# Optimization experiments

Hardware: AMD Instinct MI355X
Metric: run time of the kernel (lower is better)

The kernel has to match this reference:

```python
import jax, jax.numpy as jnp
import numpy as np

N = 100000   # total nodes in batch
E = 200000   # total edges
G = 4000     # number of graphs
H = 128      # gin_size = gin_hidden = gin_mlp_hidden = linear_hidden
L = 2        # gin_layers


def setup_inputs() -> dict:
    key = jax.random.key(0)
    ks = jax.random.split(key, 24)
    rn = lambda i, shape, s=0.05: (jax.random.normal(ks[i], shape, jnp.float32) * s)
    inp = dict(
        x=rn(0, (N, 14), 1.0),
        edge_attr=rn(1, (E, 4), 1.0),
        edge_index=jax.random.randint(ks[2], (2, E), 0, N, dtype=jnp.int32),
        batch=jnp.sort(jax.random.randint(ks[3], (N,), 0, G, dtype=jnp.int32)),
        node_w=rn(4, (14, H)), node_b=jnp.zeros((H,), jnp.float32),
        edge_w=rn(5, (4, H)), edge_b=jnp.zeros((H,), jnp.float32),
        eps=jnp.zeros((L,), jnp.float32),
        gin_w1=rn(6, (L, H, H)), gin_b1=jnp.zeros((L, H), jnp.float32),
        gin_w2=rn(7, (L, H, H)), gin_b2=jnp.zeros((L, H), jnp.float32),
        em_w1=rn(8, (L, H, H)), em_b1=jnp.zeros((L, H), jnp.float32),
        em_w2=rn(9, (L, H, H)), em_b2=jnp.zeros((L, H), jnp.float32),
        gru_wih=rn(10, (3 * H, H)), gru_whh=rn(11, (3 * H, H)),
        gru_bih=jnp.zeros((3 * H,), jnp.float32), gru_bhh=jnp.zeros((3 * H,), jnp.float32),
        lstm_wih=rn(12, (4 * H, 2 * H)), lstm_whh=rn(13, (4 * H, H)),
        lstm_bih=jnp.zeros((4 * H,), jnp.float32), lstm_bhh=jnp.zeros((4 * H,), jnp.float32),
        fc_w1=rn(14, (2 * H, H)), fc_b1=jnp.zeros((H,), jnp.float32),
        fc_w2=rn(15, (H, 1)), fc_b2=jnp.zeros((1,), jnp.float32),
    )
    return inp


def reference(x, edge_attr, edge_index, batch,
              node_w, node_b, edge_w, edge_b, eps,
              gin_w1, gin_b1, gin_w2, gin_b2,
              em_w1, em_b1, em_w2, em_b2,
              gru_wih, gru_whh, gru_bih, gru_bhh,
              lstm_wih, lstm_whh, lstm_bih, lstm_bhh,
              fc_w1, fc_b1, fc_w2, fc_b2):
    src, dst = edge_index[0], edge_index[1]
    node = x @ node_w + node_b          # [N,H]
    edge = edge_attr @ edge_w + edge_b  # [E,H]
    h = node                            # GRU hidden state
    for l in range(L):
        # GINEConv: msg = relu(x_src + e), scatter-add to dst, (1+eps)*x + agg, then MLP
        msg = jax.nn.relu(node[src] + edge)                     # [E,H] gather
        agg = jax.ops.segment_sum(msg, dst, num_segments=N)     # [N,H] scatter-add
        z = (1.0 + eps[l]) * node + agg
        m = jax.nn.relu(z @ gin_w1[l] + gin_b1[l]) @ gin_w2[l] + gin_b2[l]
        # GRU cell (seq_len=1)
        gi = m @ gru_wih.T + gru_bih
        gh = h @ gru_whh.T + gru_bhh
        ir, iz, inn = jnp.split(gi, 3, axis=-1)
        hr, hz, hn = jnp.split(gh, 3, axis=-1)
        r = jax.nn.sigmoid(ir + hr)
        zt = jax.nn.sigmoid(iz + hz)
        n = jnp.tanh(inn + r * hn)
        h = (1.0 - zt) * n + zt * h
        node = h
        # edge feature update MLP
        edge = jax.nn.relu(edge @ em_w1[l] + em_b1[l]) @ em_w2[l] + em_b2[l]
    # Set2Set pooling, processing_steps=3
    qs = jnp.zeros((G, 2 * H), node.dtype)
    hl = jnp.zeros((G, H), node.dtype)
    cl = jnp.zeros((G, H), node.dtype)
    for _ in range(3):
        g = qs @ lstm_wih.T + lstm_bih + hl @ lstm_whh.T + lstm_bhh
        i_, f_, g_, o_ = jnp.split(g, 4, axis=-1)
        cl = jax.nn.sigmoid(f_) * cl + jax.nn.sigmoid(i_) * jnp.tanh(g_)
        hl = jax.nn.sigmoid(o_) * jnp.tanh(cl)
        q = hl                                                   # [G,H]
        e = jnp.sum(node * q[batch], axis=-1)                    # [N]
        emax = jax.ops.segment_max(e, batch, num_segments=G)
        ex = jnp.exp(e - emax[batch])
        denom = jax.ops.segment_sum(ex, batch, num_segments=G)
        a = ex / jnp.maximum(denom, 1e-9)[batch]                 # per-graph softmax
        r = jax.ops.segment_sum(a[:, None] * node, batch, num_segments=G)  # [G,H]
        qs = jnp.concatenate([q, r], axis=-1)                    # [G,2H]
    out = jax.nn.relu(qs @ fc_w1 + fc_b1) @ fc_w2 + fc_b2
    return out.reshape(-1)
```

## Files before the change

kernel.cpp:

```cpp
#include <hip/hip_runtime.h>
#include <hip/hip_bf16.h>

constexpr int TN = 100000;
constexpr int TE = 200000;
constexpr int TG = 4000;
constexpr int TH = 128;

using short8 = __attribute__((ext_vector_type(8))) short;
using f32x4  = __attribute__((ext_vector_type(4))) float;
typedef __hip_bfloat16 bf16;

#define DEVINL __device__ __forceinline__
DEVINL float sigm(float x)  { return 1.f / (1.f + __expf(-x)); }
DEVINL float ftanh(float x) { return 1.f - 2.f / (__expf(2.f * x) + 1.f); }
DEVINL void unpack8(uint4 v, float* f) {
    const ushort* u = (const ushort*)&v;
#pragma unroll
    for (int j = 0; j < 8; ++j) f[j] = __bfloat162float(*(const bf16*)&u[j]);
}

__global__ void convAll(const float* __restrict__ g1, const float* __restrict__ g2,
                        const float* __restrict__ e1, const float* __restrict__ e2,
                        const float* __restrict__ gwih, const float* __restrict__ gwhh,
                        const float* __restrict__ lwih, const float* __restrict__ lwhh,
                        bf16* __restrict__ w6, bf16* __restrict__ wgru,
                        bf16* __restrict__ wl) {
    int i = blockIdx.x * 256 + threadIdx.x;
    if (i < 6 * TH * TH) {
        int m = i >> 14, r = i & 16383;
        int n = r >> 7, k = r & 127;
        const float* s = (m == 0) ? g1 : (m == 1) ? g1 + TH * TH
                       : (m == 2) ? g2 : (m == 3) ? g2 + TH * TH
                       : (m == 4) ? e1 : e2;
        w6[i] = __float2bfloat16(s[k * TH + n]);
        return;
    }
    i -= 6 * TH * TH;
    if (i < 2 * 384 * TH) {
        const float* s = (i < 384 * TH) ? gwih : gwhh;
        int r = (i < 384 * TH) ? i : i - 384 * TH;
        wgru[i] = __float2bfloat16(s[r]);
        return;
    }
    i -= 2 * 384 * TH;
    if (i < 512 * 256) {
        int c = i >> 8, k = i & 255;
        float v = (k < 128) ? lwih[c * 256 + k] + lwhh[c * 128 + k] : lwih[c * 256 + k];
        wl[i] = __float2bfloat16(v);
    }
}

template<int K>
__global__ __launch_bounds__(256) void proj64(const float* __restrict__ X,
                                              const float* __restrict__ W,
                                              const float* __restrict__ b,
                                              ushort* __restrict__ out, int M) {
    __shared__ float xs[64][K];
    int tid = threadIdx.x;
    int bm = blockIdx.x * 64;
    for (int i = tid; i < 64 * K; i += 256) {
        int r = i / K, k = i % K;
        xs[r][k] = (bm + r < M) ? X[(size_t)(bm + r) * K + k] : 0.f;
    }
    __syncthreads();
    int rb = tid >> 4, h0 = (tid & 15) * 8;
    float acc[4][8];
#pragma unroll
    for (int j = 0; j < 4; ++j)
#pragma unroll
        for (int c = 0; c < 8; ++c) acc[j][c] = b[h0 + c];
#pragma unroll
    for (int k = 0; k < K; ++k) {
        float4 w0 = *(const float4*)(W + k * TH + h0);
        float4 w1 = *(const float4*)(W + k * TH + h0 + 4);
#pragma unroll
        for (int j = 0; j < 4; ++j) {
            float xv = xs[rb + 16 * j][k];
            acc[j][0] = fmaf(xv, w0.x, acc[j][0]); acc[j][1] = fmaf(xv, w0.y, acc[j][1]);
            acc[j][2] = fmaf(xv, w0.z, acc[j][2]); acc[j][3] = fmaf(xv, w0.w, acc[j][3]);
            acc[j][4] = fmaf(xv, w1.x, acc[j][4]); acc[j][5] = fmaf(xv, w1.y, acc[j][5]);
            acc[j][6] = fmaf(xv, w1.z, acc[j][6]); acc[j][7] = fmaf(xv, w1.w, acc[j][7]);
        }
    }
#pragma unroll
    for (int j = 0; j < 4; ++j) {
        int row = bm + rb + 16 * j;
        if (row >= M) continue;
        ushort o[8];
#pragma unroll
        for (int c = 0; c < 8; ++c) {
            bf16 v = __float2bfloat16(acc[j][c]);
            o[c] = *(ushort*)&v;
        }
        *(uint4*)(out + (size_t)row * TH + h0) = *(uint4*)o;
    }
}

__global__ __launch_bounds__(256) void proj_scatter(
    const float* __restrict__ X, const float* __restrict__ W,
    const float* __restrict__ b, const int* __restrict__ perm,
    ushort* __restrict__ out, int M) {
    __shared__ float xs[64][4];
    int tid = threadIdx.x;
    int bm = blockIdx.x * 64;
    if (tid < 64) {
        float4 a = make_float4(0.f, 0.f, 0.f, 0.f);
        if (bm + tid < M) a = *(const float4*)(X + (size_t)(bm + tid) * 4);
        xs[tid][0] = a.x; xs[tid][1] = a.y; xs[tid][2] = a.z; xs[tid][3] = a.w;
    }
    __syncthreads();
    int rb = tid >> 4, h0 = (tid & 15) * 8;
    float acc[4][8];
#pragma unroll
    for (int j = 0; j < 4; ++j)
#pragma unroll
        for (int c = 0; c < 8; ++c) acc[j][c] = b[h0 + c];
#pragma unroll
    for (int k = 0; k < 4; ++k) {
        float4 w0 = *(const float4*)(W + k * TH + h0);
        float4 w1 = *(const float4*)(W + k * TH + h0 + 4);
#pragma unroll
        for (int j = 0; j < 4; ++j) {
            float xv = xs[rb + 16 * j][k];
            acc[j][0] = fmaf(xv, w0.x, acc[j][0]); acc[j][1] = fmaf(xv, w0.y, acc[j][1]);
            acc[j][2] = fmaf(xv, w0.z, acc[j][2]); acc[j][3] = fmaf(xv, w0.w, acc[j][3]);
            acc[j][4] = fmaf(xv, w1.x, acc[j][4]); acc[j][5] = fmaf(xv, w1.y, acc[j][5]);
            acc[j][6] = fmaf(xv, w1.z, acc[j][6]); acc[j][7] = fmaf(xv, w1.w, acc[j][7]);
        }
    }
#pragma unroll
    for (int j = 0; j < 4; ++j) {
        int row = bm + rb + 16 * j;
        if (row >= M) continue;
        ushort o[8];
#pragma unroll
        for (int c = 0; c < 8; ++c) {
            bf16 v = __float2bfloat16(acc[j][c]);
            o[c] = *(ushort*)&v;
        }
        *(uint4*)(out + (size_t)perm[row] * TH + h0) = *(uint4*)o;
    }
}

__global__ void count_deg(const int* __restrict__ ei_dst, int* __restrict__ deg, int En) {
    int e = blockIdx.x * 256 + threadIdx.x;
    if (e < En) atomicAdd(&deg[ei_dst[e]], 1);
}
__global__ void scan_block(const int* __restrict__ deg, int* __restrict__ rowptr,
                           int* __restrict__ bsum, int Nn) {
    __shared__ int sm[256];
    int tid = threadIdx.x;
    int gid = blockIdx.x * 256 + tid;
    int v = (gid < Nn) ? deg[gid] : 0;
    int x = v;
    sm[tid] = x; __syncthreads();
    for (int off = 1; off < 256; off <<= 1) {
        int t = (tid >= off) ? sm[tid - off] : 0;
        __syncthreads();
        x += t; sm[tid] = x;
        __syncthreads();
    }
    if (gid < Nn) rowptr[gid] = x - v;
    if (tid == 255) bsum[blockIdx.x] = x;
}
__global__ void scan_bsum(const int* __restrict__ bsum, int* __restrict__ bsumx, int nb) {
    __shared__ int sm[512];
    int tid = threadIdx.x;
    int v = (tid < nb) ? bsum[tid] : 0;
    int x = v;
    sm[tid] = x; __syncthreads();
    for (int off = 1; off < 512; off <<= 1) {
        int t = (tid >= off) ? sm[tid - off] : 0;
        __syncthreads();
        x += t; sm[tid] = x;
        __syncthreads();
    }
    if (tid < nb) bsumx[tid] = x - v;
}
__global__ void add_off(int* __restrict__ rowptr, const int* __restrict__ bsumx,
                        int Nn, int Etot) {
    int gid = blockIdx.x * 256 + threadIdx.x;
    if (gid < Nn) rowptr[gid] += bsumx[gid >> 8];
    if (gid == 0) rowptr[Nn] = Etot;
}
__global__ void fill_csr(const int* __restrict__ ei_src, const int* __restrict__ ei_dst,
                         const int* __restrict__ rowptr, int* __restrict__ cur,
                         int* __restrict__ srcp, int* __restrict__ epos, int En) {
    int e = blockIdx.x * 256 + threadIdx.x;
    if (e >= En) return;
    int d = ei_dst[e];
    int p = atomicAdd(&cur[d], 1);
    int slot = rowptr[d] + p;
    srcp[slot] = ei_src[e];
    epos[e] = slot;
}
__global__ void build_gptr(const int* __restrict__ batch, int* __restrict__ gptr,
                           int Nn, int Gn) {
    int n = blockIdx.x * 256 + threadIdx.x;
    if (n >= Nn) return;
    int bc = batch[n];
    int bp = (n == 0) ? -1 : batch[n - 1];
    for (int g = bp + 1; g <= bc; ++g) gptr[g] = n;
    if (n == Nn - 1) for (int g = bc + 1; g <= Gn; ++g) gptr[g] = Nn;
}

__global__ __launch_bounds__(256) void aggregate_v8(
    const ushort* __restrict__ node, const ushort* __restrict__ ef,
    const int* __restrict__ srcp, const int* __restrict__ rowptr,
    const float* __restrict__ eps, int l, ushort* __restrict__ zb, int Nn) {
    int t = blockIdx.x * 256 + threadIdx.x;
    int n = t >> 4;
    if (n >= Nn) return;
    int c8 = (t & 15) * 8;
    float se = 1.f + eps[l];
    float acc[8];
    uint4 nv = *(const uint4*)(node + (size_t)n * TH + c8);
    unpack8(nv, acc);
#pragma unroll
    for (int j = 0; j < 8; ++j) acc[j] *= se;
    int s0 = rowptr[n], s1 = rowptr[n + 1];
    int i = s0;
    for (; i + 1 < s1; i += 2) {
        int sa = srcp[i], sb = srcp[i + 1];
        uint4 av0 = *(const uint4*)(node + (size_t)sa * TH + c8);
        uint4 bv0 = *(const uint4*)(ef + (size_t)i * TH + c8);
        uint4 av1 = *(const uint4*)(node + (size_t)sb * TH + c8);
        uint4 bv1 = *(const uint4*)(ef + (size_t)(i + 1) * TH + c8);
        float a0[8], b0[8], a1[8], b1[8];
        unpack8(av0, a0); unpack8(bv0, b0);
        unpack8(av1, a1); unpack8(bv1, b1);
#pragma unroll
        for (int j = 0; j < 8; ++j)
            acc[j] += fmaxf(a0[j] + b0[j], 0.f) + fmaxf(a1[j] + b1[j], 0.f);
    }
    if (i < s1) {
        int sa = srcp[i];
        uint4 av = *(const uint4*)(node + (size_t)sa * TH + c8);
        uint4 bv = *(const uint4*)(ef + (size_t)i * TH + c8);
        float af[8], bf[8];
        unpack8(av, af); unpack8(bv, bf);
#pragma unroll
        for (int j = 0; j < 8; ++j) acc[j] += fmaxf(af[j] + bf[j], 0.f);
    }
    ushort o[8];
#pragma unroll
    for (int j = 0; j < 8; ++j) {
        bf16 v = __float2bfloat16(acc[j]);
        o[j] = *(ushort*)&v;
    }
    *(uint4*)(zb + (size_t)n * TH + c8) = *(uint4*)o;
}

__global__ __launch_bounds__(256) void mlp2_fused(
    const ushort* __restrict__ A, const ushort* __restrict__ W1t,
    const float* __restrict__ b1, const ushort* __restrict__ W2t,
    const float* __restrict__ b2, ushort* __restrict__ C, int M)
{
    __shared__ ushort As[128 * 128];
    const int tid = threadIdx.x;
    const int bm = blockIdx.x * 128;
    const int lane = tid & 63, w = tid >> 6;
    const int lr = lane & 15, lq = lane >> 4;
    const int wm = (w & 1) * 64, wn = (w >> 1) * 64;
    short8 wf[4][4];
#pragma unroll
    for (int ni = 0; ni < 4; ++ni)
#pragma unroll
        for (int ks = 0; ks < 4; ++ks)
            wf[ni][ks] = *(const short8*)(W1t + (size_t)(wn + ni * 16 + lr) * 128 + ks * 32 + lq * 8);
#pragma unroll
    for (int p = 0; p < 8; ++p) {
        int ch = p * 256 + tid;
        int r = ch >> 4, c = ch & 15;
        int row = bm + r;
        uint4 v = make_uint4(0u, 0u, 0u, 0u);
        if (row < M) v = *(const uint4*)(A + (size_t)row * 128 + c * 8);
        *(uint4*)(&As[r * 128 + ((c ^ (r & 15)) * 8)]) = v;
    }
    __syncthreads();
    f32x4 acc[4][4] = {};
#pragma unroll
    for (int ks = 0; ks < 4; ++ks) {
        int cb = ks * 4 + lq;
        short8 af[4];
#pragma unroll
        for (int mi = 0; mi < 4; ++mi)
            af[mi] = *(const short8*)(&As[(wm + mi * 16 + lr) * 128 + ((cb ^ lr) * 8)]);
#pragma unroll
        for (int mi = 0; mi < 4; ++mi)
#pragma unroll
            for (int ni = 0; ni < 4; ++ni)
                acc[mi][ni] = __builtin_amdgcn_mfma_f32_16x16x32_bf16(af[mi], wf[ni][ks], acc[mi][ni], 0, 0, 0);
    }
    __syncthreads();
#pragma unroll
    for (int mi = 0; mi < 4; ++mi)
#pragma unroll
        for (int reg = 0; reg < 4; ++reg) {
            int row = wm + mi * 16 + lq * 4 + reg;
#pragma unroll
            for (int ni = 0; ni < 4; ++ni) {
                int col = wn + ni * 16 + lr;
                float v = fmaxf(acc[mi][ni][reg] + b1[col], 0.f);
                bf16 bv = __float2bfloat16(v);
                As[row * 128 + (((col >> 3) ^ (row & 15)) * 8) + (col & 7)] = *(ushort*)&bv;
            }
        }
#pragma unroll
    for (int ni = 0; ni < 4; ++ni)
#pragma unroll
        for (int ks = 0; ks < 4; ++ks)
            wf[ni][ks] = *(const short8*)(W2t + (size_t)(wn + ni * 16 + lr) * 128 + ks * 32 + lq * 8);
    __syncthreads();
    {
        f32x4 acc2[4][4] = {};
#pragma unroll
        for (int ks = 0; ks < 4; ++ks) {
            int cb = ks * 4 + lq;
            short8 af[4];
#pragma unroll
            for (int mi = 0; mi < 4; ++mi)
                af[mi] = *(const short8*)(&As[(wm + mi * 16 + lr) * 128 + ((cb ^ lr) * 8)]);
#pragma unroll
            for (int mi = 0; mi < 4; ++mi)
#pragma unroll
                for (int ni = 0; ni < 4; ++ni)
                    acc2[mi][ni] = __builtin_amdgcn_mfma_f32_16x16x32_bf16(af[mi], wf[ni][ks], acc2[mi][ni], 0, 0, 0);
        }
#pragma unroll
        for (int mi = 0; mi < 4; ++mi)
#pragma unroll
            for (int reg = 0; reg < 4; ++reg) {
                int row = bm + wm + mi * 16 + lq * 4 + reg;
                if (row >= M) continue;
#pragma unroll
                for (int ni = 0; ni < 4; ++ni) {
                    int col = wn + ni * 16 + lr;
                    bf16 bv = __float2bfloat16(acc2[mi][ni][reg] + b2[col]);
                    C[(size_t)row * 128 + col] = *(ushort*)&bv;
                }
            }
    }
}

__global__ __launch_bounds__(256) void gru_fused(
    const ushort* __restrict__ mfeat, const ushort* __restrict__ wih,
    const ushort* __restrict__ whh, const float* __restrict__ bih,
    const float* __restrict__ bhh, ushort* __restrict__ node, int Nn)
{
    __shared__ ushort Ms[64 * 128];
    __shared__ ushort Hs[64 * 128];
    const int tid = threadIdx.x;
    const int bm = blockIdx.x * 64;
#pragma unroll
    for (int p = 0; p < 8; ++p) {
        int ch = p * 256 + tid;
        bool isH = ch >= 1024;
        int rc = ch & 1023;
        int r = rc >> 4, c = rc & 15;
        int row = bm + r;
        uint4 v = make_uint4(0u, 0u, 0u, 0u);
        if (row < Nn) v = *(const uint4*)((isH ? node : mfeat) + (size_t)row * 128 + c * 8);
        ushort* dst = isH ? Hs : Ms;
        *(uint4*)(&dst[r * 128 + ((c ^ (r & 15)) * 8)]) = v;
    }
    __syncthreads();
    const int lane = tid & 63, w = tid >> 6;
    const int lr = lane & 15, lq = lane >> 4;
#pragma unroll
    for (int cg = 0; cg < 2; ++cg) {
        const int col = w * 32 + cg * 16 + lr;
        f32x4 aR[4] = {}, aZ[4] = {}, aN[4] = {}, aH[4] = {};
#pragma unroll
        for (int ks = 0; ks < 4; ++ks) {
            int koff = ks * 32 + lq * 8;
            short8 wv0 = *(const short8*)(wih + (size_t)col * 128 + koff);
            short8 wv1 = *(const short8*)(wih + (size_t)(128 + col) * 128 + koff);
            short8 wv2 = *(const short8*)(wih + (size_t)(256 + col) * 128 + koff);
            short8 wv3 = *(const short8*)(whh + (size_t)col * 128 + koff);
            short8 wv4 = *(const short8*)(whh + (size_t)(128 + col) * 128 + koff);
            short8 wv5 = *(const short8*)(whh + (size_t)(256 + col) * 128 + koff);
            int cb = ks * 4 + lq;
#pragma unroll
            for (int rt = 0; rt < 4; ++rt) {
                int off = (rt * 16 + lr) * 128 + ((cb ^ lr) * 8);
                short8 am = *(const short8*)(&Ms[off]);
                short8 ah = *(const short8*)(&Hs[off]);
                aR[rt] = __builtin_amdgcn_mfma_f32_16x16x32_bf16(am, wv0, aR[rt], 0, 0, 0);
                aR[rt] = __builtin_amdgcn_mfma_f32_16x16x32_bf16(ah, wv3, aR[rt], 0, 0, 0);
                aZ[rt] = __builtin_amdgcn_mfma_f32_16x16x32_bf16(am, wv1, aZ[rt], 0, 0, 0);
                aZ[rt] = __builtin_amdgcn_mfma_f32_16x16x32_bf16(ah, wv4, aZ[rt], 0, 0, 0);
                aN[rt] = __builtin_amdgcn_mfma_f32_16x16x32_bf16(am, wv2, aN[rt], 0, 0, 0);
                aH[rt] = __builtin_amdgcn_mfma_f32_16x16x32_bf16(ah, wv5, aH[rt], 0, 0, 0);
            }
        }
        float br  = bih[col] + bhh[col];
        float bz  = bih[128 + col] + bhh[128 + col];
        float bin = bih[256 + col], bhn = bhh[256 + col];
#pragma unroll
        for (int rt = 0; rt < 4; ++rt)
#pragma unroll
            for (int reg = 0; reg < 4; ++reg) {
                int lrow = rt * 16 + lq * 4 + reg;
                int row = bm + lrow;
                if (row >= Nn) continue;
                float r = sigm(aR[rt][reg] + br);
                float z = sigm(aZ[rt][reg] + bz);
                float n = ftanh(aN[rt][reg] + bin + r * (aH[rt][reg] + bhn));
                int hofs = lrow * 128 + (((col >> 3) ^ (lrow & 15)) * 8) + (col & 7);
                float hold = __bfloat162float(*(const bf16*)&Hs[hofs]);
                bf16 hv = __float2bfloat16((1.f - z) * n + z * hold);
                node[(size_t)row * 128 + col] = *(ushort*)&hv;
            }
    }
}

__global__ __launch_bounds__(256) void lstm_fused(
    ushort* __restrict__ s, const ushort* __restrict__ Wl,
    const float* __restrict__ bih, const float* __restrict__ bhh,
    float* __restrict__ cl, int Gn)
{
    __shared__ ushort Ss[16 * 256];
    const int tid = threadIdx.x;
    const int bm = blockIdx.x * 16;
#pragma unroll
    for (int p = 0; p < 2; ++p) {
        int ch = p * 256 + tid;
        int r = ch >> 5, c = ch & 31;
        int row = bm + r;
        uint4 v = make_uint4(0u, 0u, 0u, 0u);
        if (row < Gn) v = *(const uint4*)(s + (size_t)row * 256 + c * 8);
        *(uint4*)(&Ss[r * 256 + ((c ^ (r & 15)) * 8)]) = v;
    }
    __syncthreads();
    const int lane = tid & 63, w = tid >> 6;
    const int lr = lane & 15, lq = lane >> 4;
    f32x4 acc[4][2] = {};
#pragma unroll
    for (int ks = 0; ks < 8; ++ks) {
        int cb = ks * 4 + lq;
        short8 am = *(const short8*)(&Ss[lr * 256 + ((cb ^ lr) * 8)]);
        int koff = ks * 32 + lq * 8;
#pragma unroll
        for (int g = 0; g < 4; ++g)
#pragma unroll
            for (int sub = 0; sub < 2; ++sub) {
                int col = g * 128 + w * 32 + sub * 16 + lr;
                short8 bf = *(const short8*)(Wl + (size_t)col * 256 + koff);
                acc[g][sub] = __builtin_amdgcn_mfma_f32_16x16x32_bf16(am, bf, acc[g][sub], 0, 0, 0);
            }
    }
#pragma unroll
    for (int sub = 0; sub < 2; ++sub) {
        int h = w * 32 + sub * 16 + lr;
        float bi = bih[h] + bhh[h];
        float bff = bih[128 + h] + bhh[128 + h];
        float bg = bih[256 + h] + bhh[256 + h];
        float bo = bih[384 + h] + bhh[384 + h];
#pragma unroll
        for (int reg = 0; reg < 4; ++reg) {
            int row = bm + lq * 4 + reg;
            if (row >= Gn) continue;
            float iv = sigm(acc[0][sub][reg] + bi);
            float fv = sigm(acc[1][sub][reg] + bff);
            float gv = ftanh(acc[2][sub][reg] + bg);
            float ov = sigm(acc[3][sub][reg] + bo);
            float c = fv * cl[(size_t)row * 128 + h] + iv * gv;
            cl[(size_t)row * 128 + h] = c;
            bf16 hv = __float2bfloat16(ov * ftanh(c));
            s[(size_t)row * 256 + h] = *(ushort*)&hv;
        }
    }
}

__global__ __launch_bounds__(256) void att_fused(
    const ushort* __restrict__ node, ushort* __restrict__ s,
    const int* __restrict__ gptr)
{
    __shared__ float q[128];
    __shared__ float es[512];
    __shared__ float red[8];
    __shared__ float part[16][128];
    int g = blockIdx.x;
    int tid = threadIdx.x, lane = tid & 63, wid = tid >> 6;
    int n0 = gptr[g], n1 = gptr[g + 1];
    int cnt = n1 - n0; if (cnt > 512) cnt = 512;
    if (tid < 128) q[tid] = __bfloat162float(((const bf16*)s)[(size_t)g * 256 + tid]);
    __syncthreads();
    int gr = tid >> 4, c8 = (tid & 15) * 8;
    for (int i0 = 0; i0 < cnt; i0 += 16) {
        int i = i0 + gr;
        float p = 0.f;
        if (i < cnt) {
            uint4 v = *(const uint4*)(node + (size_t)(n0 + i) * TH + c8);
            float f[8]; unpack8(v, f);
#pragma unroll
            for (int j = 0; j < 8; ++j) p = fmaf(f[j], q[c8 + j], p);
        }
        p += __shfl_down(p, 8, 16);
        p += __shfl_down(p, 4, 16);
        p += __shfl_down(p, 2, 16);
        p += __shfl_down(p, 1, 16);
        if ((tid & 15) == 0 && i < cnt) es[i] = p;
    }
    __syncthreads();
    float m = -1e30f;
    for (int i = tid; i < cnt; i += 256) m = fmaxf(m, es[i]);
    for (int off = 32; off; off >>= 1) m = fmaxf(m, __shfl_down(m, off));
    if (lane == 0) red[wid] = m;
    __syncthreads();
    m = fmaxf(fmaxf(red[0], red[1]), fmaxf(red[2], red[3]));
    float sm = 0.f;
    for (int i = tid; i < cnt; i += 256) { float ex = __expf(es[i] - m); es[i] = ex; sm += ex; }
    for (int off = 32; off; off >>= 1) sm += __shfl_down(sm, off);
    if (lane == 0) red[4 + wid] = sm;
    __syncthreads();
    sm = red[4] + red[5] + red[6] + red[7];
    float inv = 1.f / fmaxf(sm, 1e-9f);
    float racc[8] = {};
    for (int i = gr; i < cnt; i += 16) {
        uint4 v = *(const uint4*)(node + (size_t)(n0 + i) * TH + c8);
        float f[8]; unpack8(v, f);
        float a = es[i];
#pragma unroll
        for (int j = 0; j < 8; ++j) racc[j] = fmaf(a, f[j], racc[j]);
    }
#pragma unroll
    for (int j = 0; j < 8; ++j) part[gr][c8 + j] = racc[j];
    __syncthreads();
    if (tid < 128) {
        float r = 0.f;
#pragma unroll
        for (int k = 0; k < 16; ++k) r += part[k][tid];
        bf16 rv = __float2bfloat16(r * inv);
        s[(size_t)g * 256 + 128 + tid] = *(ushort*)&rv;
    }
}

__global__ __launch_bounds__(128) void final_fc(const ushort* __restrict__ s,
                                                const float* __restrict__ w1,
                                                const float* __restrict__ b1,
                                                const float* __restrict__ w2,
                                                const float* __restrict__ b2,
                                                float* __restrict__ out) {
    __shared__ float q[256];
    __shared__ float red[2];
    int g = blockIdx.x, t = threadIdx.x;
    q[t] = __bfloat162float(((const bf16*)s)[(size_t)g * 256 + t]);
    q[t + 128] = __bfloat162float(((const bf16*)s)[(size_t)g * 256 + 128 + t]);
    __syncthreads();
    float acc = b1[t];
    for (int k = 0; k < 256; ++k) acc = fmaf(q[k], w1[k * TH + t], acc);
    acc = fmaxf(acc, 0.f);
    float p = acc * w2[t];
    for (int off = 32; off; off >>= 1) p += __shfl_down(p, off);
    if ((t & 63) == 0) red[t >> 6] = p;
    __syncthreads();
    if (t == 0) out[g] = red[0] + red[1] + b2[0];
}

static void launch_mlp2(const void* A, const bf16* W1t, const float* b1,
                        const bf16* W2t, const float* b2, void* C, int M, hipStream_t s) {
    hipLaunchKernelGGL(mlp2_fused, dim3((M + 127) / 128), dim3(256), 0, s,
                       (const ushort*)A, (const ushort*)W1t, b1, (const ushort*)W2t, b2,
                       (ushort*)C, M);
}

extern "C" void kernel_launch(void* const* d_in, const int* in_sizes, int n_in,
                              void* d_out, int out_size, void* d_ws, size_t ws_size,
                              hipStream_t stream) {
    const float* x         = (const float*)d_in[0];
    const float* edge_attr = (const float*)d_in[1];
    const int*   edge_index= (const int*)d_in[2];
    const int*   batch     = (const int*)d_in[3];
    const float* node_w    = (const float*)d_in[4];
    const float* node_b    = (const float*)d_in[5];
    const float* edge_w    = (const float*)d_in[6];
    const float* edge_b    = (const float*)d_in[7];
    const float* eps       = (const float*)d_in[8];
    const float* gin_w1    = (const float*)d_in[9];
    const float* gin_b1    = (const float*)d_in[10];
    const float* gin_w2    = (const float*)d_in[11];
    const float* gin_b2    = (const float*)d_in[12];
    const float* em_w1     = (const float*)d_in[13];
    const float* em_b1     = (const float*)d_in[14];
    const float* em_w2     = (const float*)d_in[15];
    const float* em_b2     = (const float*)d_in[16];
    const float* gru_wih   = (const float*)d_in[17];
    const float* gru_whh   = (const float*)d_in[18];
    const float* gru_bih   = (const float*)d_in[19];
    const float* gru_bhh   = (const float*)d_in[20];
    const float* lstm_wih  = (const float*)d_in[21];
    const float* lstm_whh  = (const float*)d_in[22];
    const float* lstm_bih  = (const float*)d_in[23];
    const float* lstm_bhh  = (const float*)d_in[24];
    const float* fc_w1     = (const float*)d_in[25];
    const float* fc_b1     = (const float*)d_in[26];
    const float* fc_w2     = (const float*)d_in[27];
    const float* fc_b2     = (const float*)d_in[28];
    float* out = (float*)d_out;
    const int* ei_src = edge_index;
    const int* ei_dst = edge_index + TE;

    char* base = (char*)d_ws;
    size_t off = 0;
    auto alloc = [&](size_t bytes) { void* p = base + off; off += (bytes + 15) & ~size_t(15); return p; };
    bf16*  nodeb = (bf16*)alloc((size_t)TN * TH * 2);
    bf16*  zb    = (bf16*)alloc((size_t)TN * TH * 2);
    bf16*  e1b   = (bf16*)alloc((size_t)TE * TH * 2);
    int*   deg   = (int*)alloc((size_t)TN * 4);
    int*   rowptr= (int*)alloc((size_t)(TN + 1) * 4);
    int*   cur   = (int*)alloc((size_t)TN * 4);
    int*   srcp  = (int*)alloc((size_t)TE * 4);
    int*   epos  = (int*)alloc((size_t)TE * 4);
    int*   bsum  = (int*)alloc(512 * 4);
    int*   bsumx = (int*)alloc(512 * 4);
    int*   gptr  = (int*)alloc((size_t)(TG + 1) * 4);
    bf16*  w6    = (bf16*)alloc(6 * TH * TH * 2);
    bf16*  wgru  = (bf16*)alloc(2 * 384 * TH * 2);
    bf16*  wl    = (bf16*)alloc(512 * 256 * 2);
    if (ws_size < off) return;

    bf16* w_gin1_0 = w6;
    bf16* w_gin1_1 = w6 + 1 * TH * TH;
    bf16* w_gin2_0 = w6 + 2 * TH * TH;
    bf16* w_gin2_1 = w6 + 3 * TH * TH;
    bf16* w_em1    = w6 + 4 * TH * TH;
    bf16* w_em2    = w6 + 5 * TH * TH;
    bf16* w_wih    = wgru;
    bf16* w_whh    = wgru + 384 * TH;

    ushort* sbuf = (ushort*)e1b;
    float*  cl   = (float*)(sbuf + (size_t)TG * 256);

    hipMemsetAsync(deg, 0, (size_t)TN * 4, stream);
    hipMemsetAsync(cur, 0, (size_t)TN * 4, stream);
    count_deg<<<(TE + 255) / 256, 256, 0, stream>>>(ei_dst, deg, TE);
    int nb = (TN + 255) / 256;
    scan_block<<<nb, 256, 0, stream>>>(deg, rowptr, bsum, TN);
    scan_bsum<<<1, 512, 0, stream>>>(bsum, bsumx, nb);
    add_off<<<nb, 256, 0, stream>>>(rowptr, bsumx, TN, TE);
    fill_csr<<<(TE + 255) / 256, 256, 0, stream>>>(ei_src, ei_dst, rowptr, cur, srcp, epos, TE);
    build_gptr<<<(TN + 255) / 256, 256, 0, stream>>>(batch, gptr, TN, TG);

    int convTot = 6 * TH * TH + 2 * 384 * TH + 512 * 256;
    convAll<<<(convTot + 255) / 256, 256, 0, stream>>>(
        gin_w1, gin_w2, em_w1, em_w2, gru_wih, gru_whh, lstm_wih, lstm_whh,
        w6, wgru, wl);

    proj64<14><<<(TN + 63) / 64, 256, 0, stream>>>(x, node_w, node_b, (ushort*)nodeb, TN);
    proj_scatter<<<(TE + 63) / 64, 256, 0, stream>>>(edge_attr, edge_w, edge_b,
                                                     epos, (ushort*)e1b, TE);

    aggregate_v8<<<(TN * 16 + 255) / 256, 256, 0, stream>>>(
        (const ushort*)nodeb, (const ushort*)e1b, srcp, rowptr, eps, 0, (ushort*)zb, TN);
    launch_mlp2(zb, w_gin1_0, gin_b1, w_gin2_0, gin_b2, zb, TN, stream);
    gru_fused<<<(TN + 63) / 64, 256, 0, stream>>>(
        (const ushort*)zb, (const ushort*)w_wih, (const ushort*)w_whh,
        gru_bih, gru_bhh, (ushort*)nodeb, TN);

    launch_mlp2(e1b, w_em1, em_b1, w_em2, em_b2, e1b, TE, stream);
    aggregate_v8<<<(TN * 16 + 255) / 256, 256, 0, stream>>>(
        (const ushort*)nodeb, (const ushort*)e1b, srcp, rowptr, eps, 1, (ushort*)zb, TN);
    launch_mlp2(zb, w_gin1_1, gin_b1 + TH, w_gin2_1, gin_b2 + TH, zb, TN, stream);
    gru_fused<<<(TN + 63) / 64, 256, 0, stream>>>(
        (const ushort*)zb, (const ushort*)w_wih, (const ushort*)w_whh,
        gru_bih, gru_bhh, (ushort*)nodeb, TN);

    hipMemsetAsync(sbuf, 0, (size_t)TG * 256 * 2 + (size_t)TG * 128 * 4, stream);
    for (int st = 0; st < 3; ++st) {
        lstm_fused<<<(TG + 15) / 16, 256, 0, stream>>>(
            sbuf, (const ushort*)wl, lstm_bih, lstm_bhh, cl, TG);
        att_fused<<<TG, 256, 0, stream>>>((const ushort*)nodeb, sbuf, gptr);
    }

    final_fc<<<TG, 128, 0, stream>>>(sbuf, fc_w1, fc_b1, fc_w2, fc_b2, out);
}
```

Before: 590.0 us.

## Use direct global-to-LDS loads and retile GRU to 128-row 1024-thread blocks

The row-tile staging in mlp2_fused and gru_fused now uses the global_load_lds builtin, which writes straight into shared memory. The XOR swizzle moves to the global address side, so data no longer passes through registers. gru_fused is also retiled: 128 rows per block with 16 waves, each wave covering 16 columns by 64 rows, which halves the block count and changes how the weights are reused. The row bounds checks on the loads are dropped, so the last partial tile reads past the end of the input buffers, and the larger LDS footprint and block size may lower occupancy.

```diff
diff --git a/kernel.cpp b/kernel.cpp
--- a/kernel.cpp
+++ b/kernel.cpp
@@ -17,6 +17,12 @@
     const ushort* u = (const ushort*)&v;
 #pragma unroll
     for (int j = 0; j < 8; ++j) f[j] = __bfloat162float(*(const bf16*)&u[j]);
+}
+
+DEVINL void gload_lds16(const ushort* gsrc, ushort* ldst) {
+    __builtin_amdgcn_global_load_lds(
+        (const __attribute__((address_space(1))) void*)gsrc,
+        (__attribute__((address_space(3))) void*)ldst, 16, 0, 0);
 }
 
 __global__ void convAll(const float* __restrict__ g1, const float* __restrict__ g2,
@@ -269,13 +275,11 @@
         for (int ks = 0; ks < 4; ++ks)
             wf[ni][ks] = *(const short8*)(W1t + (size_t)(wn + ni * 16 + lr) * 128 + ks * 32 + lq * 8);
 #pragma unroll
-    for (int p = 0; p < 8; ++p) {
-        int ch = p * 256 + tid;
-        int r = ch >> 4, c = ch & 15;
-        int row = bm + r;
-        uint4 v = make_uint4(0u, 0u, 0u, 0u);
-        if (row < M) v = *(const uint4*)(A + (size_t)row * 128 + c * 8);
-        *(uint4*)(&As[r * 128 + ((c ^ (r & 15)) * 8)]) = v;
+    for (int i = 0; i < 8; ++i) {
+        int s = w * 512 + i * 64 + lane;
+        int r = s >> 4;
+        int c = (s & 15) ^ (r & 15);
+        gload_lds16(A + (size_t)(bm + r) * 128 + c * 8, As + (w * 512 + i * 64) * 8);
     }
     __syncthreads();
     f32x4 acc[4][4] = {};
@@ -343,57 +347,56 @@
     }
 }
 
-__global__ __launch_bounds__(256) void gru_fused(
+__global__ __launch_bounds__(1024) void gru_fused(
     const ushort* __restrict__ mfeat, const ushort* __restrict__ wih,
     const ushort* __restrict__ whh, const float* __restrict__ bih,
     const float* __restrict__ bhh, ushort* __restrict__ node, int Nn)
 {
-    __shared__ ushort Ms[64 * 128];
-    __shared__ ushort Hs[64 * 128];
+    __shared__ ushort Ms[128 * 128];
+    __shared__ ushort Hs[128 * 128];
     const int tid = threadIdx.x;
-    const int bm = blockIdx.x * 64;
-#pragma unroll
-    for (int p = 0; p < 8; ++p) {
-        int ch = p * 256 + tid;
-        bool isH = ch >= 1024;
-        int rc = ch & 1023;
-        int r = rc >> 4, c = rc & 15;
-        int row = bm + r;
-        uint4 v = make_uint4(0u, 0u, 0u, 0u);
-        if (row < Nn) v = *(const uint4*)((isH ? node : mfeat) + (size_t)row * 128 + c * 8);
-        ushort* dst = isH ? Hs : Ms;
-        *(uint4*)(&dst[r * 128 + ((c ^ (r & 15)) * 8)]) = v;
-    }
-    __syncthreads();
-    const int lane = tid & 63, w = tid >> 6;
+    const int bm = blockIdx.x * 128;
+    const int lane = tid & 63, wv = tid >> 6;
+#pragma unroll
+    for (int i = 0; i < 2; ++i) {
+        int sb = wv * 128 + i * 64;
+        int s = sb + lane;
+        int r = s >> 4;
+        int c = (s & 15) ^ (r & 15);
+        size_t goff = (size_t)(bm + r) * 128 + c * 8;
+        gload_lds16(mfeat + goff, Ms + sb * 8);
+        gload_lds16(node + goff, Hs + sb * 8);
+    }
+    __syncthreads();
     const int lr = lane & 15, lq = lane >> 4;
-#pragma unroll
-    for (int cg = 0; cg < 2; ++cg) {
-        const int col = w * 32 + cg * 16 + lr;
-        f32x4 aR[4] = {}, aZ[4] = {}, aN[4] = {}, aH[4] = {};
-#pragma unroll
-        for (int ks = 0; ks < 4; ++ks) {
-            int koff = ks * 32 + lq * 8;
-            short8 wv0 = *(const short8*)(wih + (size_t)col * 128 + koff);
-            short8 wv1 = *(const short8*)(wih + (size_t)(128 + col) * 128 + koff);
-            short8 wv2 = *(const short8*)(wih + (size_t)(256 + col) * 128 + koff);
-            short8 wv3 = *(const short8*)(whh + (size_t)col * 128 + koff);
-            short8 wv4 = *(const short8*)(whh + (size_t)(128 + col) * 128 + koff);
-            short8 wv5 = *(const short8*)(whh + (size_t)(256 + col) * 128 + koff);
-            int cb = ks * 4 + lq;
-#pragma unroll
-            for (int rt = 0; rt < 4; ++rt) {
-                int off = (rt * 16 + lr) * 128 + ((cb ^ lr) * 8);
-                short8 am = *(const short8*)(&Ms[off]);
-                short8 ah = *(const short8*)(&Hs[off]);
-                aR[rt] = __builtin_amdgcn_mfma_f32_16x16x32_bf16(am, wv0, aR[rt], 0, 0, 0);
-                aR[rt] = __builtin_amdgcn_mfma_f32_16x16x32_bf16(ah, wv3, aR[rt], 0, 0, 0);
-                aZ[rt] = __builtin_amdgcn_mfma_f32_16x16x32_bf16(am, wv1, aZ[rt], 0, 0, 0);
-                aZ[rt] = __builtin_amdgcn_mfma_f32_16x16x32_bf16(ah, wv4, aZ[rt], 0, 0, 0);
-                aN[rt] = __builtin_amdgcn_mfma_f32_16x16x32_bf16(am, wv2, aN[rt], 0, 0, 0);
-                aH[rt] = __builtin_amdgcn_mfma_f32_16x16x32_bf16(ah, wv5, aH[rt], 0, 0, 0);
-            }
-        }
+    const int cg = wv & 7, rh = wv >> 3;
+    const int col = cg * 16 + lr;
+    const int rbase = rh * 64;
+    f32x4 aR[4] = {}, aZ[4] = {}, aN[4] = {}, aH[4] = {};
+#pragma unroll
+    for (int ks = 0; ks < 4; ++ks) {
+        int koff = ks * 32 + lq * 8;
+        short8 wv0 = *(const short8*)(wih + (size_t)col * 128 + koff);
+        short8 wv1 = *(const short8*)(wih + (size_t)(128 + col) * 128 + koff);
+        short8 wv2 = *(const short8*)(wih + (size_t)(256 + col) * 128 + koff);
+        short8 wv3 = *(const short8*)(whh + (size_t)col * 128 + koff);
+        short8 wv4 = *(const short8*)(whh + (size_t)(128 + col) * 128 + koff);
+        short8 wv5 = *(const short8*)(whh + (size_t)(256 + col) * 128 + koff);
+        int cb = ks * 4 + lq;
+#pragma unroll
+        for (int rt = 0; rt < 4; ++rt) {
+            int off = (rbase + rt * 16 + lr) * 128 + ((cb ^ lr) * 8);
+            short8 am = *(const short8*)(&Ms[off]);
+            short8 ah = *(const short8*)(&Hs[off]);
+            aR[rt] = __builtin_amdgcn_mfma_f32_16x16x32_bf16(am, wv0, aR[rt], 0, 0, 0);
+            aR[rt] = __builtin_amdgcn_mfma_f32_16x16x32_bf16(ah, wv3, aR[rt], 0, 0, 0);
+            aZ[rt] = __builtin_amdgcn_mfma_f32_16x16x32_bf16(am, wv1, aZ[rt], 0, 0, 0);
+            aZ[rt] = __builtin_amdgcn_mfma_f32_16x16x32_bf16(ah, wv4, aZ[rt], 0, 0, 0);
+            aN[rt] = __builtin_amdgcn_mfma_f32_16x16x32_bf16(am, wv2, aN[rt], 0, 0, 0);
+            aH[rt] = __builtin_amdgcn_mfma_f32_16x16x32_bf16(ah, wv5, aH[rt], 0, 0, 0);
+        }
+    }
+    {
         float br  = bih[col] + bhh[col];
         float bz  = bih[128 + col] + bhh[128 + col];
         float bin = bih[256 + col], bhn = bhh[256 + col];
@@ -401,7 +404,7 @@
         for (int rt = 0; rt < 4; ++rt)
 #pragma unroll
             for (int reg = 0; reg < 4; ++reg) {
-                int lrow = rt * 16 + lq * 4 + reg;
+                int lrow = rbase + rt * 16 + lq * 4 + reg;
                 int row = bm + lrow;
                 if (row >= Nn) continue;
                 float r = sigm(aR[rt][reg] + br);
@@ -655,7 +658,7 @@
     aggregate_v8<<<(TN * 16 + 255) / 256, 256, 0, stream>>>(
         (const ushort*)nodeb, (const ushort*)e1b, srcp, rowptr, eps, 0, (ushort*)zb, TN);
     launch_mlp2(zb, w_gin1_0, gin_b1, w_gin2_0, gin_b2, zb, TN, stream);
-    gru_fused<<<(TN + 63) / 64, 256, 0, stream>>>(
+    gru_fused<<<(TN + 127) / 128, 1024, 0, stream>>>(
         (const ushort*)zb, (const ushort*)w_wih, (const ushort*)w_whh,
         gru_bih, gru_bhh, (ushort*)nodeb, TN);
 
@@ -663,7 +666,7 @@
     aggregate_v8<<<(TN * 16 + 255) / 256, 256, 0, stream>>>(
         (const ushort*)nodeb, (const ushort*)e1b, srcp, rowptr, eps, 1, (ushort*)zb, TN);
     launch_mlp2(zb, w_gin1_1, gin_b1 + TH, w_gin2_1, gin_b2 + TH, zb, TN, stream);
-    gru_fused<<<(TN + 63) / 64, 256, 0, stream>>>(
+    gru_fused<<<(TN + 127) / 128, 1024, 0, stream>>>(
         (const ushort*)zb, (const ushort*)w_wih, (const ushort*)w_whh,
         gru_bih, gru_bhh, (ushort*)nodeb, TN);
 
```

After: 581.4 us. Within noise of the previous version (-1.5%).
